# Kernel optimization log

Measured on AMD Instinct MI355X. Metric: run time of the kernel, lower is better.

## Reference

```python
import jax, jax.numpy as jnp
import numpy as np

N = 20000      # num nodes
E = 320000     # num edges (avg degree 16)
T = 12         # timesteps
IN = 128       # in_channels
GH = 64        # gnn_hidden_dim
RH = 128       # rnn_hidden_dim
OUT = 1        # out_channels


def setup_inputs() -> dict:
    key = jax.random.key(0)
    ks = jax.random.split(key, 8)
    x_seq = jax.random.normal(ks[0], (T, N, IN), jnp.float32)
    edge_index = jax.random.randint(ks[1], (2, E), 0, N, jnp.int32)
    init = lambda k, shape, fan: jax.random.normal(k, shape, jnp.float32) / np.sqrt(fan).astype(np.float32)
    gcn_w = init(ks[2], (IN, GH), IN)
    gcn_b = jnp.zeros((GH,), jnp.float32)
    w_ih = init(ks[3], (4 * RH, GH), GH)   # torch LSTM gate order: i, f, g, o
    w_hh = init(ks[4], (4 * RH, RH), RH)
    b_ih = jnp.zeros((4 * RH,), jnp.float32)
    b_hh = jnp.zeros((4 * RH,), jnp.float32)
    fc_w = init(ks[5], (OUT, RH), RH)
    fc_b = jnp.zeros((OUT,), jnp.float32)
    return {"x_seq": x_seq, "edge_index": edge_index, "gcn_w": gcn_w, "gcn_b": gcn_b,
            "w_ih": w_ih, "w_hh": w_hh, "b_ih": b_ih, "b_hh": b_hh,
            "fc_w": fc_w, "fc_b": fc_b}


def _gcn_norm(edge_index, n_nodes, dtype):
    # Add self loops, then symmetric normalization D^{-1/2} (A+I) D^{-1/2}.
    loop = jnp.arange(n_nodes, dtype=edge_index.dtype)
    src = jnp.concatenate([edge_index[0], loop])
    dst = jnp.concatenate([edge_index[1], loop])
    deg = jax.ops.segment_sum(jnp.ones(src.shape[0], dtype), dst, num_segments=n_nodes)
    dinv = jnp.where(deg > 0, jax.lax.rsqrt(deg), jnp.zeros((), dtype))
    norm = dinv[src] * dinv[dst]  # [E+N]
    return src, dst, norm


def reference(x_seq, edge_index, gcn_w, gcn_b, w_ih, w_hh, b_ih, b_hh, fc_w, fc_b):
    n_nodes = x_seq.shape[1]
    src, dst, norm = _gcn_norm(edge_index, n_nodes, x_seq.dtype)

    def gcn_step(_, x):  # x: [N, IN]
        h = x @ gcn_w                                  # [N, GH] transform first (GH < IN)
        msg = h[src] * norm[:, None]                   # gather + normalize: [E+N, GH]
        out = jax.ops.segment_sum(msg, dst, num_segments=n_nodes) + gcn_b
        return None, out

    _, hs = jax.lax.scan(gcn_step, None, x_seq)        # [T, N, GH]

    bias = b_ih + b_hh

    def lstm_step(carry, x):  # x: [N, GH]
        h, c = carry
        gates = x @ w_ih.T + h @ w_hh.T + bias         # [N, 4*RH]
        i, f, g, o = jnp.split(gates, 4, axis=-1)
        i = jax.nn.sigmoid(i)
        f = jax.nn.sigmoid(f)
        g = jnp.tanh(g)
        o = jax.nn.sigmoid(o)
        c = f * c + i * g
        h = o * jnp.tanh(c)
        return (h, c), None

    h0 = jnp.zeros((n_nodes, w_hh.shape[1]), x_seq.dtype)
    (h_last, _), _ = jax.lax.scan(lstm_step, (h0, h0), hs)
    return h_last @ fc_w.T + fc_b                      # [N, OUT]
```

## Files before the change

kernel.cpp:

```cpp
#include <hip/hip_runtime.h>

constexpr int NN = 20000;
constexpr int NE = 320000;
constexpr int TT = 12;
constexpr int CIN = 128;
constexpr int GH = 64;
constexpr int RH = 128;
constexpr int TOTAL = TT * NN;

typedef __attribute__((ext_vector_type(8))) short short8;
typedef __attribute__((ext_vector_type(4))) float f32x4;

__device__ __forceinline__ float rcp_fast(float x) { return __builtin_amdgcn_rcpf(x); }
__device__ __forceinline__ float sigf(float x) { return rcp_fast(1.0f + __expf(-x)); }
__device__ __forceinline__ float tanh_fast(float x) { return 1.0f - 2.0f * rcp_fast(__expf(2.0f * x) + 1.0f); }

__device__ __forceinline__ unsigned short f2b_rn(float x) {
    union { float f; unsigned int u; } v; v.f = x;
    unsigned int r = v.u + 0x7FFFu + ((v.u >> 16) & 1u);
    return (unsigned short)(r >> 16);
}
__device__ __forceinline__ float b2f_lo(unsigned int u) {
    union { unsigned int u; float f; } v; v.u = u << 16;
    return v.f;
}
__device__ __forceinline__ float b2f_hi(unsigned int u) {
    union { unsigned int u; float f; } v; v.u = u & 0xFFFF0000u;
    return v.f;
}

__device__ __forceinline__ void gload_lds16(const void* g, void* l) {
    __builtin_amdgcn_global_load_lds((const __attribute__((address_space(1))) void*)g,
                                     (__attribute__((address_space(3))) void*)l, 16, 0, 0);
}


__global__ __launch_bounds__(256) void degree_kernel(const int* __restrict__ dst, int* __restrict__ deg) {
    int e = blockIdx.x * blockDim.x + threadIdx.x;
    if (e < NE) atomicAdd(&deg[dst[e]], 1);
}

__global__ __launch_bounds__(256) void dinv_kernel(const int* __restrict__ deg, float* __restrict__ dinv) {
    int n = blockIdx.x * blockDim.x + threadIdx.x;
    if (n < NN) dinv[n] = rsqrtf((float)deg[n] + 1.0f);
}

__global__ __launch_bounds__(1024) void scan_kernel(const int* __restrict__ deg, int* __restrict__ row_ptr,
                                                    int* __restrict__ cursor) {
    __shared__ int sums[1024];
    int t = threadIdx.x;
    const int per = (NN + 1023) / 1024;
    int start = t * per;
    int end = min(start + per, NN);
    int s = 0;
    for (int i = start; i < end; ++i) s += deg[i];
    sums[t] = s;
    __syncthreads();
    for (int off = 1; off < 1024; off <<= 1) {
        int v = (t >= off) ? sums[t - off] : 0;
        __syncthreads();
        sums[t] += v;
        __syncthreads();
    }
    int run = (t == 0) ? 0 : sums[t - 1];
    for (int i = start; i < end; ++i) {
        row_ptr[i] = run;
        cursor[i] = run;
        run += deg[i];
    }
    if (t == 1023) row_ptr[NN] = sums[1023];
}

__global__ __launch_bounds__(256) void scatter_kernel(const int* __restrict__ src, const int* __restrict__ dst,
                                                      const float* __restrict__ dinv, int* __restrict__ cursor,
                                                      int* __restrict__ csr_src, float* __restrict__ csr_norm) {
    int e = blockIdx.x * blockDim.x + threadIdx.x;
    if (e >= NE) return;
    int d = dst[e], s = src[e];
    int pos = atomicAdd(&cursor[d], 1);
    csr_src[pos] = s;
    csr_norm[pos] = dinv[s] * dinv[d];
}


__global__ __launch_bounds__(256) void wprep_lstm_kernel(const float* __restrict__ w_ih, const float* __restrict__ w_hh,
                                                         unsigned short* __restrict__ wp) {
    int gidx = blockIdx.x * blockDim.x + threadIdx.x;
    if (gidx >= 6 * 512 * 4) return;
    int gs = gidx & 3;
    int col = (gidx >> 2) & 511;
    int chunk = gidx >> 11;
    int g = gs ^ ((col >> 1) & 3);
    int k0 = chunk * 32 + g * 8;
    short8 v;
#pragma unroll
    for (int j = 0; j < 8; ++j) {
        int k = k0 + j;
        float f = (k < 64) ? w_ih[col * 64 + k] : w_hh[col * 128 + (k - 64)];
        v[j] = (short)f2b_rn(f);
    }
    *reinterpret_cast<short8*>(wp + (size_t)gidx * 8) = v;
}

__global__ __launch_bounds__(256) void wprep_gcn_kernel(const float* __restrict__ gcn_w, unsigned short* __restrict__ wx) {
    int gidx = blockIdx.x * blockDim.x + threadIdx.x;
    if (gidx >= 4 * 64 * 4) return;
    int gs = gidx & 3;
    int col = (gidx >> 2) & 63;
    int chunk = gidx >> 8;
    int g = gs ^ ((col >> 1) & 3);
    int k0 = chunk * 32 + g * 8;
    short8 v;
#pragma unroll
    for (int j = 0; j < 8; ++j) v[j] = (short)f2b_rn(gcn_w[(k0 + j) * 64 + col]);
    *reinterpret_cast<short8*>(wx + (size_t)gidx * 8) = v;
}

__global__ __launch_bounds__(256) void bias_kernel(const float* __restrict__ b_ih, const float* __restrict__ b_hh,
                                                   float* __restrict__ bias) {
    int i = blockIdx.x * blockDim.x + threadIdx.x;
    if (i < 4 * RH) bias[i] = b_ih[i] + b_hh[i];
}


__global__ __launch_bounds__(256) void xw_mfma_kernel(const float* __restrict__ x,
                                                      const unsigned short* __restrict__ wx,
                                                      unsigned short* __restrict__ xwb) {
    __shared__ __align__(16) char As[4 * 4096];
    __shared__ __align__(16) char Bs[4 * 4096];
    int tid = threadIdx.x;
    int lane = tid & 63, w = tid >> 6;
    int m0 = blockIdx.x * 64;

#pragma unroll
    for (int j = 0; j < 4; ++j) {
        const unsigned short* src = wx + (size_t)(w * 4 + j) * 512 + lane * 8;
        gload_lds16(src, Bs + (w * 4 + j) * 1024);
    }
    {
        int row = tid >> 2, gs = tid & 3;
        int srow = m0 + row;
        int g = gs ^ ((row >> 1) & 3);
        const float* sp = x + (size_t)srow * CIN + g * 8;
#pragma unroll
        for (int c = 0; c < 4; ++c) {
            float4 f0 = *reinterpret_cast<const float4*>(sp + c * 32);
            float4 f1 = *reinterpret_cast<const float4*>(sp + c * 32 + 4);
            short8 v;
            v[0] = (short)f2b_rn(f0.x); v[1] = (short)f2b_rn(f0.y);
            v[2] = (short)f2b_rn(f0.z); v[3] = (short)f2b_rn(f0.w);
            v[4] = (short)f2b_rn(f1.x); v[5] = (short)f2b_rn(f1.y);
            v[6] = (short)f2b_rn(f1.z); v[7] = (short)f2b_rn(f1.w);
            *reinterpret_cast<short8*>(As + c * 4096 + row * 64 + gs * 16) = v;
        }
    }
    __syncthreads();

    f32x4 acc[4] = {};
    int rl = w * 16 + (lane & 15);
    int o = lane >> 4;
#pragma unroll
    for (int c = 0; c < 4; ++c) {
        int gsa = o ^ ((rl >> 1) & 3);
        short8 a = *reinterpret_cast<const short8*>(As + c * 4096 + rl * 64 + gsa * 16);
#pragma unroll
        for (int cn = 0; cn < 4; ++cn) {
            int col = cn * 16 + (lane & 15);
            int gsb = o ^ ((col >> 1) & 3);
            short8 b = *reinterpret_cast<const short8*>(Bs + c * 4096 + col * 64 + gsb * 16);
            acc[cn] = __builtin_amdgcn_mfma_f32_16x16x32_bf16(a, b, acc[cn], 0, 0, 0);
        }
    }
#pragma unroll
    for (int cn = 0; cn < 4; ++cn)
#pragma unroll
        for (int r = 0; r < 4; ++r) {
            int row = m0 + w * 16 + (lane >> 4) * 4 + r;
            int col = cn * 16 + (lane & 15);
            xwb[(size_t)row * GH + col] = f2b_rn(acc[cn][r]);
        }
}


__global__ __launch_bounds__(256) void gather_kernel(const unsigned short* __restrict__ xwb, const float* __restrict__ dinv,
                                                     const int* __restrict__ row_ptr, const int* __restrict__ csr_src,
                                                     const float* __restrict__ csr_norm, const float* __restrict__ gcn_b,
                                                     unsigned short* __restrict__ hs_b) {
    int t0 = blockIdx.y * 2;
    int wpair = (blockIdx.x * blockDim.x + threadIdx.x) >> 6;
    int lane = threadIdx.x & 63;
    int g = lane >> 5, sl = lane & 31;
    int node = wpair * 2 + g;
    const unsigned int* sl0 = (const unsigned int*)(xwb + (size_t)t0 * NN * GH);
    const unsigned int* sl1 = sl0 + (size_t)NN * 32;

    float dv = dinv[node];
    float b0 = gcn_b[sl * 2], b1 = gcn_b[sl * 2 + 1];
    unsigned int u0 = sl0[(size_t)node * 32 + sl];
    unsigned int u1 = sl1[(size_t)node * 32 + sl];
    float a0x = b0 + dv * dv * b2f_lo(u0);
    float a0y = b1 + dv * dv * b2f_hi(u0);
    float a1x = b0 + dv * dv * b2f_lo(u1);
    float a1y = b1 + dv * dv * b2f_hi(u1);

    int e0 = row_ptr[node];
    int deg = row_ptr[node + 1] - e0;
    int degA = __shfl(deg, 0), degB = __shfl(deg, 32);
    int dmax = max(degA, degB);

    for (int base = 0; base < dmax; base += 32) {
        int cnt = min(deg - base, 32);
        bool valid = sl < cnt;
        int myidx = valid ? csr_src[e0 + base + sl] : 0;
        float mynm = valid ? csr_norm[e0 + base + sl] : 0.f;
        int c8 = (max(cnt, 0) + 7) & ~7;
        int c8o = __shfl(c8, (1 - g) << 5);
        int c8w = max(c8, c8o);
        for (int j = 0; j < c8w; j += 8) {
            int s0 = __shfl(myidx, (g << 5) + j + 0), s1 = __shfl(myidx, (g << 5) + j + 1);
            int s2 = __shfl(myidx, (g << 5) + j + 2), s3 = __shfl(myidx, (g << 5) + j + 3);
            int s4 = __shfl(myidx, (g << 5) + j + 4), s5 = __shfl(myidx, (g << 5) + j + 5);
            int s6 = __shfl(myidx, (g << 5) + j + 6), s7 = __shfl(myidx, (g << 5) + j + 7);
            float n0 = __shfl(mynm, (g << 5) + j + 0), n1 = __shfl(mynm, (g << 5) + j + 1);
            float n2 = __shfl(mynm, (g << 5) + j + 2), n3 = __shfl(mynm, (g << 5) + j + 3);
            float n4 = __shfl(mynm, (g << 5) + j + 4), n5 = __shfl(mynm, (g << 5) + j + 5);
            float n6 = __shfl(mynm, (g << 5) + j + 6), n7 = __shfl(mynm, (g << 5) + j + 7);
            unsigned int p0 = sl0[(size_t)s0 * 32 + sl], q0 = sl1[(size_t)s0 * 32 + sl];
            unsigned int p1 = sl0[(size_t)s1 * 32 + sl], q1 = sl1[(size_t)s1 * 32 + sl];
            unsigned int p2 = sl0[(size_t)s2 * 32 + sl], q2 = sl1[(size_t)s2 * 32 + sl];
            unsigned int p3 = sl0[(size_t)s3 * 32 + sl], q3 = sl1[(size_t)s3 * 32 + sl];
            unsigned int p4 = sl0[(size_t)s4 * 32 + sl], q4 = sl1[(size_t)s4 * 32 + sl];
            unsigned int p5 = sl0[(size_t)s5 * 32 + sl], q5 = sl1[(size_t)s5 * 32 + sl];
            unsigned int p6 = sl0[(size_t)s6 * 32 + sl], q6 = sl1[(size_t)s6 * 32 + sl];
            unsigned int p7 = sl0[(size_t)s7 * 32 + sl], q7 = sl1[(size_t)s7 * 32 + sl];
            a0x += n0 * b2f_lo(p0); a0y += n0 * b2f_hi(p0); a1x += n0 * b2f_lo(q0); a1y += n0 * b2f_hi(q0);
            a0x += n1 * b2f_lo(p1); a0y += n1 * b2f_hi(p1); a1x += n1 * b2f_lo(q1); a1y += n1 * b2f_hi(q1);
            a0x += n2 * b2f_lo(p2); a0y += n2 * b2f_hi(p2); a1x += n2 * b2f_lo(q2); a1y += n2 * b2f_hi(q2);
            a0x += n3 * b2f_lo(p3); a0y += n3 * b2f_hi(p3); a1x += n3 * b2f_lo(q3); a1y += n3 * b2f_hi(q3);
            a0x += n4 * b2f_lo(p4); a0y += n4 * b2f_hi(p4); a1x += n4 * b2f_lo(q4); a1y += n4 * b2f_hi(q4);
            a0x += n5 * b2f_lo(p5); a0y += n5 * b2f_hi(p5); a1x += n5 * b2f_lo(q5); a1y += n5 * b2f_hi(q5);
            a0x += n6 * b2f_lo(p6); a0y += n6 * b2f_hi(p6); a1x += n6 * b2f_lo(q6); a1y += n6 * b2f_hi(q6);
            a0x += n7 * b2f_lo(p7); a0y += n7 * b2f_hi(p7); a1x += n7 * b2f_lo(q7); a1y += n7 * b2f_hi(q7);
        }
    }
    unsigned int o0 = (unsigned int)f2b_rn(a0x) | ((unsigned int)f2b_rn(a0y) << 16);
    unsigned int o1 = (unsigned int)f2b_rn(a1x) | ((unsigned int)f2b_rn(a1y) << 16);
    ((unsigned int*)hs_b)[((size_t)t0 * NN + node) * 32 + sl] = o0;
    ((unsigned int*)hs_b)[((size_t)(t0 + 1) * NN + node) * 32 + sl] = o1;
}


#define HS_OFF 0
#define HA_OFF 20480
#define RED_OFF 61440
#define SMEM_BYTES 64000

__global__ __launch_bounds__(512, 2) void lstm_persist_kernel(const unsigned short* __restrict__ hs_all,
                                                              const unsigned short* __restrict__ wp,
                                                              const float* __restrict__ bias,
                                                              const float* __restrict__ fc_w,
                                                              const float* __restrict__ fc_b,
                                                              float* __restrict__ out) {
    __shared__ __align__(16) char smem[SMEM_BYTES];
    int tid = threadIdx.x;
    int lane = tid & 63, w = tid >> 6;
    int l15 = lane & 15, o = lane >> 4;
    int base = blockIdx.x * 80;

    int sw = o ^ ((l15 >> 1) & 3);
    int colbase = w * 16 + l15;
    float bi = bias[colbase], bff = bias[128 + colbase], bg = bias[256 + colbase], bo = bias[384 + colbase];
    float fcw = fc_w[colbase];
    f32x4 binit[4] = {{bi, bi, bi, bi}, {bff, bff, bff, bff}, {bg, bg, bg, bg}, {bo, bo, bo, bo}};

    int h_chunk = w >> 1;
    int h_g = ((w & 1) << 1) + (l15 >> 3);
    int h_j = l15 & 7;

    short8 breg[6][4];
#pragma unroll
    for (int c = 0; c < 6; ++c)
#pragma unroll
        for (int g = 0; g < 4; ++g) {
            size_t goff = ((size_t)(c * 512 + g * 128 + colbase) * 4 + sw) * 8;
            breg[c][g] = *reinterpret_cast<const short8*>(wp + goff);
            asm volatile("" : "+v"(breg[c][g]));
        }

    {
#pragma unroll
        for (int i = 0; i < 10; ++i) ((int*)(smem + HA_OFF))[tid + i * 512] = 0;
#pragma unroll
        for (int j = 0; j < 2; ++j) {
            int gi = j * 512 + tid;
            if (gi < 640) {
                int cc = (gi >= 320) ? 1 : 0;
                int rem = gi - cc * 320;
                int row = rem >> 2, gs = rem & 3;
                int g = gs ^ ((row >> 1) & 3);
                const unsigned short* src = hs_all + ((size_t)(base + row)) * 64 + cc * 32 + g * 8;
                gload_lds16(src, smem + HS_OFF + gi * 16);
            }
        }
    }
    __syncthreads();

    float c_reg[5][4] = {};
    f32x4 acc[5][4];

#pragma unroll 1
    for (int t = 0; t < TT; ++t) {
        if (t + 1 < TT) {
            char* dstb = smem + HS_OFF + ((t + 1) & 1) * 10240;
#pragma unroll
            for (int j = 0; j < 2; ++j) {
                int gi = j * 512 + tid;
                if (gi < 640) {
                    int cc = (gi >= 320) ? 1 : 0;
                    int rem = gi - cc * 320;
                    int row = rem >> 2, gs = rem & 3;
                    int g = gs ^ ((row >> 1) & 3);
                    const unsigned short* src = hs_all + ((size_t)(t + 1) * NN + base + row) * 64 + cc * 32 + g * 8;
                    gload_lds16(src, dstb + gi * 16);
                }
            }
        }

#pragma unroll
        for (int mi = 0; mi < 5; ++mi)
#pragma unroll
            for (int g = 0; g < 4; ++g) acc[mi][g] = binit[g];

        const char* hsb = smem + HS_OFF + (t & 1) * 10240;
        const char* hab = smem + HA_OFF + (t & 1) * 20480;
        __builtin_amdgcn_s_setprio(1);
#pragma unroll
        for (int c = 0; c < 6; ++c) {
            const char* abase = (c < 2) ? (hsb + c * 5120) : (hab + (c - 2) * 5120);
            short8 a[5];
#pragma unroll
            for (int mi = 0; mi < 5; ++mi)
                a[mi] = *reinterpret_cast<const short8*>(abase + (mi * 16 + l15) * 64 + sw * 16);
#pragma unroll
            for (int g = 0; g < 4; ++g)
#pragma unroll
                for (int mi = 0; mi < 5; ++mi)
                    acc[mi][g] = __builtin_amdgcn_mfma_f32_16x16x32_bf16(a[mi], breg[c][g], acc[mi][g], 0, 0, 0);
        }
        __builtin_amdgcn_s_setprio(0);

        char* hwr = smem + HA_OFF + ((t + 1) & 1) * 20480;
        if (t + 1 < TT) {
#pragma unroll
            for (int mi = 0; mi < 5; ++mi)
#pragma unroll
                for (int r = 0; r < 4; ++r) {
                    float iv = sigf(acc[mi][0][r]);
                    float fv = sigf(acc[mi][1][r]);
                    float gv = tanh_fast(acc[mi][2][r]);
                    float ov = sigf(acc[mi][3][r]);
                    float cnew = fv * c_reg[mi][r] + iv * gv;
                    c_reg[mi][r] = cnew;
                    float hv = ov * tanh_fast(cnew);
                    int row = mi * 16 + o * 4 + r;
                    int gs_h = h_g ^ ((row >> 1) & 3);
                    *(unsigned short*)(hwr + h_chunk * 5120 + row * 64 + gs_h * 16 + h_j * 2) = f2b_rn(hv);
                }
        } else {
#pragma unroll
            for (int mi = 0; mi < 5; ++mi)
#pragma unroll
                for (int r = 0; r < 4; ++r) {
                    float iv = sigf(acc[mi][0][r]);
                    float fv = sigf(acc[mi][1][r]);
                    float gv = tanh_fast(acc[mi][2][r]);
                    float ov = sigf(acc[mi][3][r]);
                    float cnew = fv * c_reg[mi][r] + iv * gv;
                    float hv = ov * tanh_fast(cnew);
                    float p = hv * fcw;
                    p += __shfl_xor(p, 1);
                    p += __shfl_xor(p, 2);
                    p += __shfl_xor(p, 4);
                    p += __shfl_xor(p, 8);
                    if (l15 == 0) {
                        int row = mi * 16 + o * 4 + r;
                        ((float*)(smem + RED_OFF))[w * 80 + row] = p;
                    }
                }
        }
        __syncthreads();
    }

    if (tid < 80) {
        const float* red = (const float*)(smem + RED_OFF);
        float s = 0.f;
#pragma unroll
        for (int w8 = 0; w8 < 8; ++w8) s += red[w8 * 80 + tid];
        out[base + tid] = s + fc_b[0];
    }
}


extern "C" void kernel_launch(void* const* d_in, const int* in_sizes, int n_in,
                              void* d_out, int out_size, void* d_ws, size_t ws_size,
                              hipStream_t stream) {
    const float* x_seq = (const float*)d_in[0];
    const int* edge = (const int*)d_in[1];
    const float* gcn_w = (const float*)d_in[2];
    const float* gcn_b = (const float*)d_in[3];
    const float* w_ih = (const float*)d_in[4];
    const float* w_hh = (const float*)d_in[5];
    const float* b_ih = (const float*)d_in[6];
    const float* b_hh = (const float*)d_in[7];
    const float* fc_w = (const float*)d_in[8];
    const float* fc_b = (const float*)d_in[9];
    float* out = (float*)d_out;

    char* w = (char*)d_ws;
    auto carve = [&](size_t bytes) {
        void* p = (void*)w;
        w += (bytes + 255) & ~(size_t)255;
        return p;
    };
    float* dinv = (float*)carve(NN * 4);
    int* deg = (int*)carve(NN * 4);
    int* row_ptr = (int*)carve((NN + 1) * 4);
    int* cursor = (int*)carve(NN * 4);
    int* csr_src = (int*)carve(NE * 4);
    float* csr_norm = (float*)carve(NE * 4);
    unsigned short* xwb = (unsigned short*)carve((size_t)TOTAL * GH * 2);
    unsigned short* hs_b = (unsigned short*)carve((size_t)TOTAL * GH * 2);
    unsigned short* wp = (unsigned short*)carve((size_t)6 * 512 * 4 * 8 * 2);
    unsigned short* wx = (unsigned short*)carve((size_t)4 * 64 * 4 * 8 * 2);
    float* bias = (float*)carve(512 * 4);

    hipMemsetAsync(deg, 0, NN * 4, stream);

    const int* e_src = edge;
    const int* e_dst = edge + NE;

    degree_kernel<<<(NE + 255) / 256, 256, 0, stream>>>(e_dst, deg);
    dinv_kernel<<<(NN + 255) / 256, 256, 0, stream>>>(deg, dinv);
    scan_kernel<<<1, 1024, 0, stream>>>(deg, row_ptr, cursor);
    scatter_kernel<<<(NE + 255) / 256, 256, 0, stream>>>(e_src, e_dst, dinv, cursor, csr_src, csr_norm);

    wprep_lstm_kernel<<<(6 * 512 * 4 + 255) / 256, 256, 0, stream>>>(w_ih, w_hh, wp);
    wprep_gcn_kernel<<<(4 * 64 * 4 + 255) / 256, 256, 0, stream>>>(gcn_w, wx);
    bias_kernel<<<2, 256, 0, stream>>>(b_ih, b_hh, bias);

    xw_mfma_kernel<<<TOTAL / 64, 256, 0, stream>>>(x_seq, wx, xwb);
    dim3 ggrid(NN / 2 / 4, TT / 2);
    gather_kernel<<<ggrid, 256, 0, stream>>>(xwb, dinv, row_ptr, csr_src, csr_norm, gcn_b, hs_b);
    lstm_persist_kernel<<<NN / 80, 512, 0, stream>>>(hs_b, wp, bias, fc_w, fc_b, out);
}
```

Measured before the change: 231.2 us.

## Fuse GCN neighbor gather into persistent LSTM kernel with staggered warp groups

Removes the standalone gather kernel and its hs_b round trip through global memory. The persistent LSTM kernel now computes the next timestep's aggregated GCN features straight into the LDS double buffer. Half the warps do this before the MFMA gate computation and half after it, to overlap the gather latency with compute. This saves a kernel launch and HBM traffic, but puts irregular gather latency on the serial LSTM critical path with only 250 blocks, and the gather loses its earlier two-timesteps-per-index amortization.

Result: slower. 357.6 us (+54.6%).

```diff
diff --git a/kernel.cpp b/kernel.cpp
--- a/kernel.cpp
+++ b/kernel.cpp
@@ -182,85 +182,88 @@
 }
 
 
-__global__ __launch_bounds__(256) void gather_kernel(const unsigned short* __restrict__ xwb, const float* __restrict__ dinv,
-                                                     const int* __restrict__ row_ptr, const int* __restrict__ csr_src,
-                                                     const float* __restrict__ csr_norm, const float* __restrict__ gcn_b,
-                                                     unsigned short* __restrict__ hs_b) {
-    int t0 = blockIdx.y * 2;
-    int wpair = (blockIdx.x * blockDim.x + threadIdx.x) >> 6;
-    int lane = threadIdx.x & 63;
-    int g = lane >> 5, sl = lane & 31;
-    int node = wpair * 2 + g;
-    const unsigned int* sl0 = (const unsigned int*)(xwb + (size_t)t0 * NN * GH);
-    const unsigned int* sl1 = sl0 + (size_t)NN * 32;
-
-    float dv = dinv[node];
-    float b0 = gcn_b[sl * 2], b1 = gcn_b[sl * 2 + 1];
-    unsigned int u0 = sl0[(size_t)node * 32 + sl];
-    unsigned int u1 = sl1[(size_t)node * 32 + sl];
-    float a0x = b0 + dv * dv * b2f_lo(u0);
-    float a0y = b1 + dv * dv * b2f_hi(u0);
-    float a1x = b0 + dv * dv * b2f_lo(u1);
-    float a1y = b1 + dv * dv * b2f_hi(u1);
-
-    int e0 = row_ptr[node];
-    int deg = row_ptr[node + 1] - e0;
-    int degA = __shfl(deg, 0), degB = __shfl(deg, 32);
-    int dmax = max(degA, degB);
-
-    for (int base = 0; base < dmax; base += 32) {
-        int cnt = min(deg - base, 32);
-        bool valid = sl < cnt;
-        int myidx = valid ? csr_src[e0 + base + sl] : 0;
-        float mynm = valid ? csr_norm[e0 + base + sl] : 0.f;
-        int c8 = (max(cnt, 0) + 7) & ~7;
-        int c8o = __shfl(c8, (1 - g) << 5);
-        int c8w = max(c8, c8o);
-        for (int j = 0; j < c8w; j += 8) {
-            int s0 = __shfl(myidx, (g << 5) + j + 0), s1 = __shfl(myidx, (g << 5) + j + 1);
-            int s2 = __shfl(myidx, (g << 5) + j + 2), s3 = __shfl(myidx, (g << 5) + j + 3);
-            int s4 = __shfl(myidx, (g << 5) + j + 4), s5 = __shfl(myidx, (g << 5) + j + 5);
-            int s6 = __shfl(myidx, (g << 5) + j + 6), s7 = __shfl(myidx, (g << 5) + j + 7);
-            float n0 = __shfl(mynm, (g << 5) + j + 0), n1 = __shfl(mynm, (g << 5) + j + 1);
-            float n2 = __shfl(mynm, (g << 5) + j + 2), n3 = __shfl(mynm, (g << 5) + j + 3);
-            float n4 = __shfl(mynm, (g << 5) + j + 4), n5 = __shfl(mynm, (g << 5) + j + 5);
-            float n6 = __shfl(mynm, (g << 5) + j + 6), n7 = __shfl(mynm, (g << 5) + j + 7);
-            unsigned int p0 = sl0[(size_t)s0 * 32 + sl], q0 = sl1[(size_t)s0 * 32 + sl];
-            unsigned int p1 = sl0[(size_t)s1 * 32 + sl], q1 = sl1[(size_t)s1 * 32 + sl];
-            unsigned int p2 = sl0[(size_t)s2 * 32 + sl], q2 = sl1[(size_t)s2 * 32 + sl];
-            unsigned int p3 = sl0[(size_t)s3 * 32 + sl], q3 = sl1[(size_t)s3 * 32 + sl];
-            unsigned int p4 = sl0[(size_t)s4 * 32 + sl], q4 = sl1[(size_t)s4 * 32 + sl];
-            unsigned int p5 = sl0[(size_t)s5 * 32 + sl], q5 = sl1[(size_t)s5 * 32 + sl];
-            unsigned int p6 = sl0[(size_t)s6 * 32 + sl], q6 = sl1[(size_t)s6 * 32 + sl];
-            unsigned int p7 = sl0[(size_t)s7 * 32 + sl], q7 = sl1[(size_t)s7 * 32 + sl];
-            a0x += n0 * b2f_lo(p0); a0y += n0 * b2f_hi(p0); a1x += n0 * b2f_lo(q0); a1y += n0 * b2f_hi(q0);
-            a0x += n1 * b2f_lo(p1); a0y += n1 * b2f_hi(p1); a1x += n1 * b2f_lo(q1); a1y += n1 * b2f_hi(q1);
-            a0x += n2 * b2f_lo(p2); a0y += n2 * b2f_hi(p2); a1x += n2 * b2f_lo(q2); a1y += n2 * b2f_hi(q2);
-            a0x += n3 * b2f_lo(p3); a0y += n3 * b2f_hi(p3); a1x += n3 * b2f_lo(q3); a1y += n3 * b2f_hi(q3);
-            a0x += n4 * b2f_lo(p4); a0y += n4 * b2f_hi(p4); a1x += n4 * b2f_lo(q4); a1y += n4 * b2f_hi(q4);
-            a0x += n5 * b2f_lo(p5); a0y += n5 * b2f_hi(p5); a1x += n5 * b2f_lo(q5); a1y += n5 * b2f_hi(q5);
-            a0x += n6 * b2f_lo(p6); a0y += n6 * b2f_hi(p6); a1x += n6 * b2f_lo(q6); a1y += n6 * b2f_hi(q6);
-            a0x += n7 * b2f_lo(p7); a0y += n7 * b2f_hi(p7); a1x += n7 * b2f_lo(q7); a1y += n7 * b2f_hi(q7);
-        }
-    }
-    unsigned int o0 = (unsigned int)f2b_rn(a0x) | ((unsigned int)f2b_rn(a0y) << 16);
-    unsigned int o1 = (unsigned int)f2b_rn(a1x) | ((unsigned int)f2b_rn(a1y) << 16);
-    ((unsigned int*)hs_b)[((size_t)t0 * NN + node) * 32 + sl] = o0;
-    ((unsigned int*)hs_b)[((size_t)(t0 + 1) * NN + node) * 32 + sl] = o1;
-}
-
-
 #define HS_OFF 0
 #define HA_OFF 20480
 #define RED_OFF 61440
 #define SMEM_BYTES 64000
 
-__global__ __launch_bounds__(512, 2) void lstm_persist_kernel(const unsigned short* __restrict__ hs_all,
-                                                              const unsigned short* __restrict__ wp,
-                                                              const float* __restrict__ bias,
-                                                              const float* __restrict__ fc_w,
-                                                              const float* __restrict__ fc_b,
-                                                              float* __restrict__ out) {
+__device__ __forceinline__ void gather_step(const unsigned int* __restrict__ xw32,
+                                            const float* __restrict__ dinv,
+                                            const int* __restrict__ row_ptr,
+                                            const int* __restrict__ csr_src,
+                                            const float* __restrict__ csr_norm,
+                                            float b0, float b1,
+                                            char* hs_slot, int base, int w, int lane) {
+    int g = lane >> 5, sl = lane & 31;
+    int cc = sl >> 4;
+    int gsel = (sl & 15) >> 2;
+    int jj = (2 * (sl & 15)) & 7;
+#pragma unroll 1
+    for (int pr = 0; pr < 5; ++pr) {
+        int lrow = w * 10 + pr * 2 + g;
+        int node = base + lrow;
+        float dv = dinv[node];
+        unsigned int u = xw32[(size_t)node * 32 + sl];
+        float ax = b0 + dv * dv * b2f_lo(u);
+        float ay = b1 + dv * dv * b2f_hi(u);
+
+        int e0 = row_ptr[node];
+        int deg = row_ptr[node + 1] - e0;
+        int degA = __shfl(deg, 0), degB = __shfl(deg, 32);
+        int dmax = max(degA, degB);
+
+        for (int bs = 0; bs < dmax; bs += 32) {
+            int cnt = min(deg - bs, 32);
+            bool valid = sl < cnt;
+            int myidx = valid ? csr_src[e0 + bs + sl] : 0;
+            float mynm = valid ? csr_norm[e0 + bs + sl] : 0.f;
+            int c8 = (max(cnt, 0) + 7) & ~7;
+            int c8o = __shfl(c8, (1 - g) << 5);
+            int c8w = max(c8, c8o);
+            for (int j = 0; j < c8w; j += 8) {
+                int s0 = __shfl(myidx, (g << 5) + j + 0), s1 = __shfl(myidx, (g << 5) + j + 1);
+                int s2 = __shfl(myidx, (g << 5) + j + 2), s3 = __shfl(myidx, (g << 5) + j + 3);
+                int s4 = __shfl(myidx, (g << 5) + j + 4), s5 = __shfl(myidx, (g << 5) + j + 5);
+                int s6 = __shfl(myidx, (g << 5) + j + 6), s7 = __shfl(myidx, (g << 5) + j + 7);
+                float n0 = __shfl(mynm, (g << 5) + j + 0), n1 = __shfl(mynm, (g << 5) + j + 1);
+                float n2 = __shfl(mynm, (g << 5) + j + 2), n3 = __shfl(mynm, (g << 5) + j + 3);
+                float n4 = __shfl(mynm, (g << 5) + j + 4), n5 = __shfl(mynm, (g << 5) + j + 5);
+                float n6 = __shfl(mynm, (g << 5) + j + 6), n7 = __shfl(mynm, (g << 5) + j + 7);
+                unsigned int p0 = xw32[(size_t)s0 * 32 + sl];
+                unsigned int p1 = xw32[(size_t)s1 * 32 + sl];
+                unsigned int p2 = xw32[(size_t)s2 * 32 + sl];
+                unsigned int p3 = xw32[(size_t)s3 * 32 + sl];
+                unsigned int p4 = xw32[(size_t)s4 * 32 + sl];
+                unsigned int p5 = xw32[(size_t)s5 * 32 + sl];
+                unsigned int p6 = xw32[(size_t)s6 * 32 + sl];
+                unsigned int p7 = xw32[(size_t)s7 * 32 + sl];
+                ax += n0 * b2f_lo(p0); ay += n0 * b2f_hi(p0);
+                ax += n1 * b2f_lo(p1); ay += n1 * b2f_hi(p1);
+                ax += n2 * b2f_lo(p2); ay += n2 * b2f_hi(p2);
+                ax += n3 * b2f_lo(p3); ay += n3 * b2f_hi(p3);
+                ax += n4 * b2f_lo(p4); ay += n4 * b2f_hi(p4);
+                ax += n5 * b2f_lo(p5); ay += n5 * b2f_hi(p5);
+                ax += n6 * b2f_lo(p6); ay += n6 * b2f_hi(p6);
+                ax += n7 * b2f_lo(p7); ay += n7 * b2f_hi(p7);
+            }
+        }
+        int gs_h = gsel ^ ((lrow >> 1) & 3);
+        unsigned int ov = (unsigned int)f2b_rn(ax) | ((unsigned int)f2b_rn(ay) << 16);
+        *(unsigned int*)(hs_slot + cc * 5120 + lrow * 64 + gs_h * 16 + jj * 2) = ov;
+    }
+}
+
+__global__ __launch_bounds__(512, 2) void lstm_fused_kernel(const unsigned short* __restrict__ xwb,
+                                                            const float* __restrict__ dinv,
+                                                            const int* __restrict__ row_ptr,
+                                                            const int* __restrict__ csr_src,
+                                                            const float* __restrict__ csr_norm,
+                                                            const float* __restrict__ gcn_b,
+                                                            const unsigned short* __restrict__ wp,
+                                                            const float* __restrict__ bias,
+                                                            const float* __restrict__ fc_w,
+                                                            const float* __restrict__ fc_b,
+                                                            float* __restrict__ out) {
     __shared__ __align__(16) char smem[SMEM_BYTES];
     int tid = threadIdx.x;
     int lane = tid & 63, w = tid >> 6;
@@ -277,6 +280,10 @@
     int h_g = ((w & 1) << 1) + (l15 >> 3);
     int h_j = l15 & 7;
 
+    int gsl = lane & 31;
+    float gb0 = gcn_b[gsl * 2], gb1 = gcn_b[gsl * 2 + 1];
+    bool gfirst = ((w >> 2) & 1);
+
     short8 breg[6][4];
 #pragma unroll
     for (int c = 0; c < 6; ++c)
@@ -287,22 +294,10 @@
             asm volatile("" : "+v"(breg[c][g]));
         }
 
-    {
-#pragma unroll
-        for (int i = 0; i < 10; ++i) ((int*)(smem + HA_OFF))[tid + i * 512] = 0;
-#pragma unroll
-        for (int j = 0; j < 2; ++j) {
-            int gi = j * 512 + tid;
-            if (gi < 640) {
-                int cc = (gi >= 320) ? 1 : 0;
-                int rem = gi - cc * 320;
-                int row = rem >> 2, gs = rem & 3;
-                int g = gs ^ ((row >> 1) & 3);
-                const unsigned short* src = hs_all + ((size_t)(base + row)) * 64 + cc * 32 + g * 8;
-                gload_lds16(src, smem + HS_OFF + gi * 16);
-            }
-        }
-    }
+#pragma unroll
+    for (int i = 0; i < 10; ++i) ((int*)(smem + HA_OFF))[tid + i * 512] = 0;
+    gather_step((const unsigned int*)xwb, dinv, row_ptr, csr_src, csr_norm,
+                gb0, gb1, smem + HS_OFF, base, w, lane);
     __syncthreads();
 
     float c_reg[5][4] = {};
@@ -310,21 +305,11 @@
 
 #pragma unroll 1
     for (int t = 0; t < TT; ++t) {
-        if (t + 1 < TT) {
-            char* dstb = smem + HS_OFF + ((t + 1) & 1) * 10240;
-#pragma unroll
-            for (int j = 0; j < 2; ++j) {
-                int gi = j * 512 + tid;
-                if (gi < 640) {
-                    int cc = (gi >= 320) ? 1 : 0;
-                    int rem = gi - cc * 320;
-                    int row = rem >> 2, gs = rem & 3;
-                    int g = gs ^ ((row >> 1) & 3);
-                    const unsigned short* src = hs_all + ((size_t)(t + 1) * NN + base + row) * 64 + cc * 32 + g * 8;
-                    gload_lds16(src, dstb + gi * 16);
-                }
-            }
-        }
+        const unsigned int* nxt32 = (const unsigned int*)(xwb + (size_t)(t + 1) * NN * GH);
+        char* hs_nxt = smem + HS_OFF + ((t + 1) & 1) * 10240;
+
+        if (gfirst && t + 1 < TT)
+            gather_step(nxt32, dinv, row_ptr, csr_src, csr_norm, gb0, gb1, hs_nxt, base, w, lane);
 
 #pragma unroll
         for (int mi = 0; mi < 5; ++mi)
@@ -388,6 +373,10 @@
                     }
                 }
         }
+
+        if (!gfirst && t + 1 < TT)
+            gather_step(nxt32, dinv, row_ptr, csr_src, csr_norm, gb0, gb1, hs_nxt, base, w, lane);
+
         __syncthreads();
     }
 
@@ -429,7 +418,6 @@
     int* csr_src = (int*)carve(NE * 4);
     float* csr_norm = (float*)carve(NE * 4);
     unsigned short* xwb = (unsigned short*)carve((size_t)TOTAL * GH * 2);
-    unsigned short* hs_b = (unsigned short*)carve((size_t)TOTAL * GH * 2);
     unsigned short* wp = (unsigned short*)carve((size_t)6 * 512 * 4 * 8 * 2);
     unsigned short* wx = (unsigned short*)carve((size_t)4 * 64 * 4 * 8 * 2);
     float* bias = (float*)carve(512 * 4);
@@ -449,7 +437,6 @@
     bias_kernel<<<2, 256, 0, stream>>>(b_ih, b_hh, bias);
 
     xw_mfma_kernel<<<TOTAL / 64, 256, 0, stream>>>(x_seq, wx, xwb);
-    dim3 ggrid(NN / 2 / 4, TT / 2);
-    gather_kernel<<<ggrid, 256, 0, stream>>>(xwb, dinv, row_ptr, csr_src, csr_norm, gcn_b, hs_b);
-    lstm_persist_kernel<<<NN / 80, 512, 0, stream>>>(hs_b, wp, bias, fc_w, fc_b, out);
-}
+    lstm_fused_kernel<<<NN / 80, 512, 0, stream>>>(xwb, dinv, row_ptr, csr_src, csr_norm, gcn_b,
+                                                   wp, bias, fc_w, fc_b, out);
+}
```
